# Kernel optimization log

Hardware: AMD Instinct MI355X
Metric: run time of the kernel (lower is better)

Reference implementation:

```python
import jax, jax.numpy as jnp
import numpy as np
from jax import lax

B, IMG, P, CIN = 8, 224, 16, 3
D, NH, E, HID, DEPTH, NC = 768, 12, 4, 3072, 12, 1000
NPAT = (IMG // P) ** 2  # 196
S = NPAT + 1            # 197 tokens incl cls
HD = D // NH            # 64
EPS = 1e-5


def _ln(x, g, b):
    m = jnp.mean(x, axis=-1, keepdims=True)
    v = jnp.mean((x - m) ** 2, axis=-1, keepdims=True)
    return (x - m) * lax.rsqrt(v + EPS) * g + b


def setup_inputs() -> dict:
    key = jax.random.key(0)
    ks = list(jax.random.split(key, 24))
    def rn(k, shape, s=0.02):
        return (jax.random.normal(k, shape) * s).astype(jnp.float32)
    inp = {
        "x": jax.random.normal(ks[0], (B, CIN, IMG, IMG), dtype=jnp.float32),
        "patch_w": rn(ks[1], (D, CIN, P, P)),
        "patch_b": jnp.zeros((D,), jnp.float32),
        "cls_token": jnp.zeros((1, 1, D), jnp.float32),
        "pos_embed": rn(ks[2], (1, S, D)),
        "ln1_g": jnp.ones((DEPTH, D), jnp.float32),
        "ln1_b": jnp.zeros((DEPTH, D), jnp.float32),
        "ln2_g": jnp.ones((DEPTH, D), jnp.float32),
        "ln2_b": jnp.zeros((DEPTH, D), jnp.float32),
        "attn_in_w": rn(ks[3], (DEPTH, 3 * D, D)),
        "attn_in_b": jnp.zeros((DEPTH, 3 * D), jnp.float32),
        "attn_out_w": rn(ks[4], (DEPTH, D, D)),
        "attn_out_b": jnp.zeros((DEPTH, D), jnp.float32),
        "gate_w": rn(ks[5], (DEPTH, E, D)),
        "gate_b": jnp.zeros((DEPTH, E), jnp.float32),
        "w1": rn(ks[6], (DEPTH, E, D, HID)),
        "b1": jnp.zeros((DEPTH, E, HID), jnp.float32),
        "w2": rn(ks[7], (DEPTH, E, HID, D)),
        "b2": jnp.zeros((DEPTH, E, D), jnp.float32),
        "head_w": rn(ks[8], (NC, D)),
        "head_b": jnp.zeros((NC,), jnp.float32),
    }
    return inp


def _forward(x, patch_w, patch_b, cls_token, pos_embed, ln1_g, ln1_b, ln2_g, ln2_b,
             attn_in_w, attn_in_b, attn_out_w, attn_out_b, gate_w, gate_b,
             w1, b1, w2, b2, head_w, head_b):
    # Patch embedding: conv stride=patch, then flatten spatial -> tokens
    feat = lax.conv_general_dilated(x, patch_w, window_strides=(P, P), padding="VALID",
                                    dimension_numbers=("NCHW", "OIHW", "NCHW"))
    t = feat.reshape(B, D, NPAT).transpose(0, 2, 1) + patch_b  # [B, 196, D]
    cls = jnp.broadcast_to(cls_token, (B, 1, D))
    h = jnp.concatenate([cls, t], axis=1) + pos_embed  # [B, S, D]

    scale = 1.0 / np.sqrt(HD).astype(np.float32)
    for i in range(DEPTH):
        # ---- attention (query = LN(x); key/value = x, as in source) ----
        qn = _ln(h, ln1_g[i], ln1_b[i])
        wq, wk, wv = attn_in_w[i, :D], attn_in_w[i, D:2 * D], attn_in_w[i, 2 * D:]
        bq, bk, bv = attn_in_b[i, :D], attn_in_b[i, D:2 * D], attn_in_b[i, 2 * D:]
        q = (qn @ wq.T + bq).reshape(B, S, NH, HD)
        k = (h @ wk.T + bk).reshape(B, S, NH, HD)
        v = (h @ wv.T + bv).reshape(B, S, NH, HD)
        scores = jnp.einsum("bqhd,bkhd->bhqk", q, k) * scale
        attn = jax.nn.softmax(scores, axis=-1)
        o = jnp.einsum("bhqk,bkhd->bqhd", attn, v).reshape(B, S, D)
        h = h + o @ attn_out_w[i].T + attn_out_b[i]

        # ---- Top-1 gated MoE MLP ----
        y = _ln(h, ln2_g[i], ln2_b[i])
        logits = y @ gate_w[i].T + gate_b[i]            # [B,S,E]
        probs = jax.nn.softmax(logits, axis=-1)
        top = jnp.argmax(probs, axis=-1)                # [B,S]
        onehot = jax.nn.one_hot(top, E, dtype=y.dtype)  # [B,S,E]
        gv = jnp.sum(probs * onehot, axis=-1)           # [B,S] top-1 gate score
        hidd = jax.nn.gelu(jnp.einsum("bsd,edh->besh", y, w1[i]) + b1[i][None, :, None, :])
        eout = jnp.einsum("besh,ehd->besd", hidd, w2[i]) + b2[i][None, :, None, :]
        moe = jnp.einsum("bse,besd->bsd", onehot, eout) * gv[..., None]
        h = h + moe

    return h[:, 0] @ head_w.T + head_b  # [B, NC]


def reference(x, patch_w, patch_b, cls_token, pos_embed, ln1_g, ln1_b, ln2_g, ln2_b,
              attn_in_w, attn_in_b, attn_out_w, attn_out_b, gate_w, gate_b,
              w1, b1, w2, b2, head_w, head_b):
    return _forward(x, patch_w, patch_b, cls_token, pos_embed, ln1_g, ln1_b, ln2_g,
                    ln2_b, attn_in_w, attn_in_b, attn_out_w, attn_out_b, gate_w,
                    gate_b, w1, b1, w2, b2, head_w, head_b)
```

## Files before the change

### kernel.cpp

```cpp
#include <hip/hip_runtime.h>
#include <math.h>


#define BB 8
#define SS 197
#define DD 768
#define MT (BB*SS)
#define NPATCH 196
#define MPE (BB*NPATCH)
#define HHID 3072
#define NEXP 4
#define QKVN 2304
#define SCW 228

typedef __bf16 bf16_t;
typedef bf16_t bf16x4 __attribute__((ext_vector_type(4)));
typedef bf16_t bf16x8 __attribute__((ext_vector_type(8)));
typedef float  f32x4  __attribute__((ext_vector_type(4)));

__device__ __forceinline__ void gload16(const bf16_t* g, bf16_t* l) {
    __builtin_amdgcn_global_load_lds(
        (const __attribute__((address_space(1))) unsigned int*)g,
        (__attribute__((address_space(3))) unsigned int*)l,
        16, 0, 0);
}

__device__ __forceinline__ bf16x8 cvt8(float4 a, float4 b) {
    bf16x8 o;
    o[0]=(bf16_t)a.x; o[1]=(bf16_t)a.y; o[2]=(bf16_t)a.z; o[3]=(bf16_t)a.w;
    o[4]=(bf16_t)b.x; o[5]=(bf16_t)b.y; o[6]=(bf16_t)b.z; o[7]=(bf16_t)b.w;
    return o;
}

__global__ void gather_patches(const float* __restrict__ x, bf16_t* __restrict__ Xp) {
    int i = blockIdx.x * 256 + threadIdx.x;
    if (i >= MPE * DD) return;
    int k = i % DD;
    int m = i / DD;
    int pw = k & 15, ph = (k >> 4) & 15, cin = k >> 8;
    int px = m % 14, py = (m / 14) % 14, b = m / NPATCH;
    int row = py * 16 + ph, col = px * 16 + pw;
    Xp[i] = (bf16_t)x[((size_t)(b * 3 + cin) * 224 + row) * 224 + col];
}

__global__ void init_misc(const float* __restrict__ cls, const float* __restrict__ pos,
                          float* __restrict__ h, bf16_t* __restrict__ hb, int* __restrict__ cnt) {
    int i = blockIdx.x * 256 + threadIdx.x;
    if (i < 12*NEXP) cnt[i] = 0;
    if (i < BB * DD) {
        int b = i / DD, d = i % DD;
        float v = cls[d] + pos[d];
        size_t o = (size_t)(b * SS) * DD + d;
        h[o] = v;
        hb[o] = (bf16_t)v;
    }
}

template<int BM, int BN, int WM, int WN, int MODE, int BL>
__global__ __launch_bounds__((BM/WM)*(BN/WN)*64) void gemm_bf16(
    const bf16_t* __restrict__ A, const bf16_t* __restrict__ A2, int nsplit,
    const float* __restrict__ Bw,
    const float* __restrict__ bias, float* __restrict__ C, bf16_t* __restrict__ Cb,
    const int* __restrict__ cnt, const int* __restrict__ idx,
    const float* __restrict__ gv, int M, int N, int K)
{
    constexpr int NW  = (BM/WM)*(BN/WN);
    constexpr int NTH = NW * 64;
    constexpr int WNC = BN/WN;
    constexpr int MI  = WM/16;
    constexpr int NI  = WN/16;
    constexpr int IA  = (BM/8)/NW;
    constexpr int BT  = (BN*8)/NTH;
    constexpr bool GATHER = (MODE == 3 || MODE == 4);

    int z = blockIdx.z;
    int count = GATHER ? cnt[z] : M;
    int m0 = blockIdx.y * BM;
    if (m0 >= count) return;
    int n0 = blockIdx.x * BN;
    if (n0 >= nsplit) A = A2;
    Bw += (size_t)z * N * K;
    const float* biasz = bias ? (bias + (size_t)z * N) : nullptr;

    __shared__ bf16_t As[2][BM * 64];
    __shared__ bf16_t Bs[2][BN * 64];
    __shared__ int toks[BM];

    int tid = threadIdx.x, lane = tid & 63, w = tid >> 6;
    if (tid < BM) {
        int mm = m0 + tid;
        if (mm > count - 1) mm = count - 1;
        toks[tid] = GATHER ? idx[z * MT + mm] : mm;
    }
    __syncthreads();

    int wm = (w / WNC) * WM, wn = (w % WNC) * WN;
    int fr = lane & 15, fs = lane >> 4;

    f32x4 acc[MI][NI];
    #pragma unroll
    for (int mi = 0; mi < MI; mi++)
        #pragma unroll
        for (int ni = 0; ni < NI; ni++)
            #pragma unroll
            for (int j = 0; j < 4; j++) acc[mi][ni][j] = 0.f;

    int nk = K >> 6;
    int srow = lane >> 3, scc = lane & 7;

    float4 bA[BT], bB[BT];
    float  bt[BT][8];

    #define A_STAGE(buf, k0)                                                            \
        {                                                                               \
            _Pragma("unroll")                                                           \
            for (int i = 0; i < IA; i++) {                                              \
                int blk = i*NW + w;                                                     \
                int row = blk*8 + srow;                                                 \
                const bf16_t* s = A + (size_t)toks[row] * K + (k0) + ((scc ^ (row & 7)) << 3); \
                gload16(s, &As[buf][blk * 512]);                                        \
            }                                                                           \
        }

    #define B_LOAD(k0)                                                                  \
        {                                                                               \
            _Pragma("unroll")                                                           \
            for (int i = 0; i < BT; i++) {                                              \
                int task = i*NTH + tid;                                                 \
                if (BL == 0) {                                                          \
                    int row = task >> 3, sl = task & 7;                                 \
                    const float* s = Bw + (size_t)(n0 + row) * K + (k0) + sl*8;         \
                    bA[i] = *(const float4*)s;                                          \
                    bB[i] = *(const float4*)(s + 4);                                    \
                } else {                                                                \
                    int n = task & (BN-1), sl = task / BN;                              \
                    const float* s = Bw + (size_t)((k0) + sl*8) * N + n0 + n;           \
                    _Pragma("unroll")                                                   \
                    for (int j = 0; j < 8; j++) bt[i][j] = s[(size_t)j * N];            \
                }                                                                       \
            }                                                                           \
        }

    #define B_WRITE(buf)                                                                \
        {                                                                               \
            _Pragma("unroll")                                                           \
            for (int i = 0; i < BT; i++) {                                              \
                int task = i*NTH + tid;                                                 \
                int row, sl;                                                            \
                bf16x8 o;                                                               \
                if (BL == 0) {                                                          \
                    row = task >> 3; sl = task & 7;                                     \
                    o = cvt8(bA[i], bB[i]);                                             \
                } else {                                                                \
                    row = task & (BN-1); sl = task / BN;                                \
                    _Pragma("unroll")                                                   \
                    for (int j = 0; j < 8; j++) o[j] = (bf16_t)bt[i][j];                \
                }                                                                       \
                *(bf16x8*)&Bs[buf][row * 64 + ((sl ^ (row & 7)) << 3)] = o;             \
            }                                                                           \
        }

    A_STAGE(0, 0);
    B_LOAD(0);
    B_WRITE(0);
    __syncthreads();
    int cur = 0;
    for (int t = 0; t < nk; t++) {
        if (t + 1 < nk) { A_STAGE(cur ^ 1, (t + 1) << 6); B_LOAD((t + 1) << 6); }
        #pragma unroll
        for (int ks = 0; ks < 2; ks++) {
            bf16x8 af[MI], bfr[NI];
            #pragma unroll
            for (int mi = 0; mi < MI; mi++) {
                int r = wm + mi * 16 + fr;
                af[mi] = *(bf16x8*)&As[cur][r * 64 + (((fs + ks*4) ^ (r & 7)) << 3)];
            }
            #pragma unroll
            for (int ni = 0; ni < NI; ni++) {
                int r = wn + ni * 16 + fr;
                bfr[ni] = *(bf16x8*)&Bs[cur][r * 64 + (((fs + ks*4) ^ (r & 7)) << 3)];
            }
            #pragma unroll
            for (int mi = 0; mi < MI; mi++)
                #pragma unroll
                for (int ni = 0; ni < NI; ni++)
                    acc[mi][ni] = __builtin_amdgcn_mfma_f32_16x16x32_bf16(af[mi], bfr[ni], acc[mi][ni], 0, 0, 0);
        }
        if (t + 1 < nk) B_WRITE(cur ^ 1);
        __syncthreads();
        cur ^= 1;
    }
    #undef A_STAGE
    #undef B_LOAD
    #undef B_WRITE

    #pragma unroll
    for (int mi = 0; mi < MI; mi++) {
        #pragma unroll
        for (int j = 0; j < 4; j++) {
            int rr = wm + mi * 16 + fs * 4 + j;
            if (m0 + rr >= count) continue;
            int crow = toks[rr];
            #pragma unroll
            for (int ni = 0; ni < NI; ni++) {
                int col = n0 + wn + ni * 16 + fr;
                float v = acc[mi][ni][j];
                if (MODE >= 2) v += biasz[col];
                if (MODE == 2) {
                    C[(size_t)crow * N + col] += v;
                } else if (MODE == 3) {
                    float g = 0.5f * v * (1.0f + tanhf(0.7978845608028654f * (v + 0.044715f * v * v * v)));
                    Cb[(size_t)crow * N + col] = (bf16_t)g;
                } else if (MODE == 4) {
                    float* p = &C[(size_t)crow * N + col];
                    float nv = *p + v * gv[crow];
                    *p = nv;
                    Cb[(size_t)crow * N + col] = (bf16_t)nv;
                } else if (MODE == 5) {
                    Cb[(size_t)crow * N + col] = (bf16_t)v;
                } else if (MODE == 7) {
                    int bb = crow / NPATCH, p = crow - bb * NPATCH;
                    size_t o = ((size_t)(bb * SS + 1 + p)) * DD + col;
                    float vv = v + gv[(size_t)(1 + p) * DD + col];
                    C[o] = vv;
                    Cb[o] = (bf16_t)vv;
                }
            }
        }
    }
}

__global__ __launch_bounds__(256) void ln1_kernel(const float* __restrict__ x,
                                                  const float* __restrict__ g,
                                                  const float* __restrict__ b,
                                                  bf16_t* __restrict__ qn)
{
    int wid = (blockIdx.x * 256 + threadIdx.x) >> 6;
    if (wid >= MT) return;
    int lane = threadIdx.x & 63;
    const float4* xr = (const float4*)(x + (size_t)wid * DD);
    float4 v0 = xr[lane], v1 = xr[lane + 64], v2 = xr[lane + 128];
    float s = v0.x+v0.y+v0.z+v0.w + v1.x+v1.y+v1.z+v1.w + v2.x+v2.y+v2.z+v2.w;
    #pragma unroll
    for (int o = 32; o > 0; o >>= 1) s += __shfl_xor(s, o);
    float mean = s * (1.0f/DD);
    float s2 = 0.f;
    #pragma unroll
    for (int c = 0; c < 3; c++) {
        float4 v = c == 0 ? v0 : (c == 1 ? v1 : v2);
        float dx = v.x-mean, dy = v.y-mean, dz = v.z-mean, dw = v.w-mean;
        s2 += dx*dx + dy*dy + dz*dz + dw*dw;
    }
    #pragma unroll
    for (int o = 32; o > 0; o >>= 1) s2 += __shfl_xor(s2, o);
    float rs = rsqrtf(s2 * (1.0f/DD) + 1e-5f);
    const float4* gr = (const float4*)g;
    const float4* br = (const float4*)b;
    #pragma unroll
    for (int c = 0; c < 3; c++) {
        float4 v = c == 0 ? v0 : (c == 1 ? v1 : v2);
        float4 gg = gr[lane + 64*c], bb = br[lane + 64*c];
        bf16x4 o;
        o[0] = (bf16_t)((v.x - mean) * rs * gg.x + bb.x);
        o[1] = (bf16_t)((v.y - mean) * rs * gg.y + bb.y);
        o[2] = (bf16_t)((v.z - mean) * rs * gg.z + bb.z);
        o[3] = (bf16_t)((v.w - mean) * rs * gg.w + bb.w);
        *(bf16x4*)(qn + (size_t)wid * DD + (lane + 64*c) * 4) = o;
    }
}

__global__ __launch_bounds__(256) void ln2_gate_kernel(const float* __restrict__ x,
                                                       const float* __restrict__ g,
                                                       const float* __restrict__ b,
                                                       const float* __restrict__ gw,
                                                       const float* __restrict__ gb,
                                                       bf16_t* __restrict__ yb,
                                                       float* __restrict__ gv,
                                                       int* __restrict__ cnt,
                                                       int* __restrict__ idxb)
{
    int wid = (blockIdx.x * 256 + threadIdx.x) >> 6;
    if (wid >= MT) return;
    int lane = threadIdx.x & 63;
    const float4* xr = (const float4*)(x + (size_t)wid * DD);
    float4 v0 = xr[lane], v1 = xr[lane + 64], v2 = xr[lane + 128];
    float s = v0.x+v0.y+v0.z+v0.w + v1.x+v1.y+v1.z+v1.w + v2.x+v2.y+v2.z+v2.w;
    #pragma unroll
    for (int o = 32; o > 0; o >>= 1) s += __shfl_xor(s, o);
    float mean = s * (1.0f/DD);
    float s2 = 0.f;
    #pragma unroll
    for (int c = 0; c < 3; c++) {
        float4 v = c == 0 ? v0 : (c == 1 ? v1 : v2);
        float dx = v.x-mean, dy = v.y-mean, dz = v.z-mean, dw = v.w-mean;
        s2 += dx*dx + dy*dy + dz*dz + dw*dw;
    }
    #pragma unroll
    for (int o = 32; o > 0; o >>= 1) s2 += __shfl_xor(s2, o);
    float rs = rsqrtf(s2 * (1.0f/DD) + 1e-5f);
    const float4* gr = (const float4*)g;
    const float4* br = (const float4*)b;
    float p0 = 0.f, p1 = 0.f, p2 = 0.f, p3 = 0.f;
    #pragma unroll
    for (int c = 0; c < 3; c++) {
        float4 v = c == 0 ? v0 : (c == 1 ? v1 : v2);
        float4 gg = gr[lane + 64*c], bb = br[lane + 64*c];
        float y0 = (v.x - mean) * rs * gg.x + bb.x;
        float y1 = (v.y - mean) * rs * gg.y + bb.y;
        float y2 = (v.z - mean) * rs * gg.z + bb.z;
        float y3 = (v.w - mean) * rs * gg.w + bb.w;
        bf16x4 o; o[0]=(bf16_t)y0; o[1]=(bf16_t)y1; o[2]=(bf16_t)y2; o[3]=(bf16_t)y3;
        *(bf16x4*)(yb + (size_t)wid * DD + (lane + 64*c) * 4) = o;
        int off = lane + 64*c;
        float4 w0 = ((const float4*)(gw          ))[off];
        float4 w1v = ((const float4*)(gw +   DD  ))[off];
        float4 w2v = ((const float4*)(gw + 2*DD  ))[off];
        float4 w3v = ((const float4*)(gw + 3*DD  ))[off];
        p0 += y0*w0.x + y1*w0.y + y2*w0.z + y3*w0.w;
        p1 += y0*w1v.x + y1*w1v.y + y2*w1v.z + y3*w1v.w;
        p2 += y0*w2v.x + y1*w2v.y + y2*w2v.z + y3*w2v.w;
        p3 += y0*w3v.x + y1*w3v.y + y2*w3v.z + y3*w3v.w;
    }
    #pragma unroll
    for (int o = 32; o > 0; o >>= 1) {
        p0 += __shfl_xor(p0, o); p1 += __shfl_xor(p1, o);
        p2 += __shfl_xor(p2, o); p3 += __shfl_xor(p3, o);
    }
    if (lane == 0) {
        float l0 = p0 + gb[0], l1 = p1 + gb[1], l2 = p2 + gb[2], l3 = p3 + gb[3];
        int top = 0; float best = l0;
        if (l1 > best) { best = l1; top = 1; }
        if (l2 > best) { best = l2; top = 2; }
        if (l3 > best) { best = l3; top = 3; }
        float Z = __expf(l0-best) + __expf(l1-best) + __expf(l2-best) + __expf(l3-best);
        gv[wid] = 1.0f / Z;
        int pos = atomicAdd(&cnt[top], 1);
        idxb[top * MT + pos] = wid;
    }
}

__global__ __launch_bounds__(256) void attn_kernel(const bf16_t* __restrict__ qkv,
                                                   bf16_t* __restrict__ ob)
{
    int qt = blockIdx.x, hh = blockIdx.y, b = blockIdx.z;
    __shared__ bf16_t Qs[64 * 64];
    __shared__ bf16_t KV[64 * 68];
    __shared__ float  Sc[64 * SCW];
    __shared__ float  linv[64];

    int tid = threadIdx.x, lane = tid & 63, w = tid >> 6;
    int wm = (w >> 1) * 32, wn = (w & 1) * 32;
    int fr = lane & 15, fs = lane >> 4;

    #pragma unroll
    for (int it = 0; it < 2; it++) {
        int row = 8*(it*4 + w) + (lane >> 3), cc = lane & 7;
        int q = qt*64 + row; if (q > SS-1) q = SS-1;
        const bf16_t* src = qkv + ((size_t)(b*SS + q))*QKVN + hh*64 + ((cc ^ (row & 7)) << 3);
        gload16(src, &Qs[(it*4 + w) * 512]);
    }

    for (int kt = 0; kt < 4; kt++) {
        __syncthreads();
        #pragma unroll
        for (int it = 0; it < 2; it++) {
            int row = 8*(it*4 + w) + (lane >> 3), cc = lane & 7;
            int k = kt*64 + row; if (k > SS-1) k = SS-1;
            const bf16_t* src = qkv + ((size_t)(b*SS + k))*QKVN + 768 + hh*64 + ((cc ^ (row & 7)) << 3);
            gload16(src, &KV[(it*4 + w) * 512]);
        }
        __syncthreads();
        f32x4 acc[2][2];
        #pragma unroll
        for (int mi = 0; mi < 2; mi++)
            #pragma unroll
            for (int ni = 0; ni < 2; ni++)
                #pragma unroll
                for (int j = 0; j < 4; j++) acc[mi][ni][j] = 0.f;
        #pragma unroll
        for (int ks = 0; ks < 2; ks++) {
            bf16x8 af[2], bfr[2];
            #pragma unroll
            for (int mi = 0; mi < 2; mi++) {
                int r = wm + mi * 16 + fr;
                af[mi] = *(bf16x8*)&Qs[r * 64 + (((fs + ks*4) ^ (r & 7)) << 3)];
            }
            #pragma unroll
            for (int ni = 0; ni < 2; ni++) {
                int r = wn + ni * 16 + fr;
                bfr[ni] = *(bf16x8*)&KV[r * 64 + (((fs + ks*4) ^ (r & 7)) << 3)];
            }
            #pragma unroll
            for (int mi = 0; mi < 2; mi++)
                #pragma unroll
                for (int ni = 0; ni < 2; ni++)
                    acc[mi][ni] = __builtin_amdgcn_mfma_f32_16x16x32_bf16(af[mi], bfr[ni], acc[mi][ni], 0, 0, 0);
        }
        #pragma unroll
        for (int mi = 0; mi < 2; mi++)
            #pragma unroll
            for (int j = 0; j < 4; j++) {
                int qr = wm + mi * 16 + fs * 4 + j;
                #pragma unroll
                for (int ni = 0; ni < 2; ni++) {
                    int col = kt*64 + wn + ni * 16 + fr;
                    if (col < SCW) {
                        float v = acc[mi][ni][j] * 0.125f;
                        if (col > SS-1) v = -1e30f;
                        Sc[qr * SCW + col] = v;
                    }
                }
            }
    }
    __syncthreads();

    {
        int row = tid >> 2, c = tid & 3;
        float m = -1e30f;
        for (int i = c; i < SCW; i += 4) m = fmaxf(m, Sc[row * SCW + i]);
        m = fmaxf(m, __shfl_xor(m, 1, 4));
        m = fmaxf(m, __shfl_xor(m, 2, 4));
        float s = 0.f;
        for (int i = c; i < SCW; i += 4) {
            float e = __expf(Sc[row * SCW + i] - m);
            Sc[row * SCW + i] = e;
            s += e;
        }
        s += __shfl_xor(s, 1, 4);
        s += __shfl_xor(s, 2, 4);
        if (c == 0) linv[row] = 1.0f / s;
    }

    f32x4 pv[2][2];
    #pragma unroll
    for (int mi = 0; mi < 2; mi++)
        #pragma unroll
        for (int ni = 0; ni < 2; ni++)
            #pragma unroll
            for (int j = 0; j < 4; j++) pv[mi][ni][j] = 0.f;

    for (int kt = 0; kt < 4; kt++) {
        __syncthreads();
        {
            int s = tid >> 2, c2 = tid & 3;
            int k = kt*64 + s; if (k > SS-1) k = SS-1;
            const bf16_t* vr = qkv + ((size_t)(b*SS + k))*QKVN + 1536 + hh*64;
            bf16x8 v0 = *(const bf16x8*)(vr + c2*16);
            bf16x8 v1 = *(const bf16x8*)(vr + c2*16 + 8);
            #pragma unroll
            for (int j = 0; j < 8; j++) {
                KV[(c2*16 + j) * 68 + s]     = v0[j];
                KV[(c2*16 + 8 + j) * 68 + s] = v1[j];
            }
        }
        __syncthreads();
        #pragma unroll
        for (int ks = 0; ks < 2; ks++) {
            int s0 = kt*64 + ks*32;
            if (s0 > SS-1) continue;
            bf16x8 af[2], bfr[2];
            #pragma unroll
            for (int mi = 0; mi < 2; mi++) {
                int qr = wm + mi * 16 + fr;
                const float* p = &Sc[qr * SCW + s0 + fs * 8];
                af[mi] = cvt8(*(const float4*)p, *(const float4*)(p + 4));
            }
            #pragma unroll
            for (int ni = 0; ni < 2; ni++) {
                int d = wn + ni * 16 + fr;
                bfr[ni] = *(bf16x8*)&KV[d * 68 + ks*32 + fs*8];
            }
            #pragma unroll
            for (int mi = 0; mi < 2; mi++)
                #pragma unroll
                for (int ni = 0; ni < 2; ni++)
                    pv[mi][ni] = __builtin_amdgcn_mfma_f32_16x16x32_bf16(af[mi], bfr[ni], pv[mi][ni], 0, 0, 0);
        }
    }

    #pragma unroll
    for (int mi = 0; mi < 2; mi++)
        #pragma unroll
        for (int j = 0; j < 4; j++) {
            int qr = wm + mi * 16 + fs * 4 + j;
            int q = qt*64 + qr;
            if (q > SS-1) continue;
            float il = linv[qr];
            #pragma unroll
            for (int ni = 0; ni < 2; ni++) {
                int d = wn + ni * 16 + fr;
                ob[((size_t)(b*SS + q))*DD + hh*64 + d] = (bf16_t)(pv[mi][ni][j] * il);
            }
        }
}

__global__ void head_kernel(const float* __restrict__ h, const float* __restrict__ hw,
                            const float* __restrict__ hb, float* __restrict__ out)
{
    int i = blockIdx.x * 256 + threadIdx.x;
    if (i >= BB * 1000) return;
    int b = i & 7, n = i >> 3;
    const float4* hr = (const float4*)(h + (size_t)(b * SS) * DD);
    const float4* wr = (const float4*)(hw + (size_t)n * DD);
    float s = 0.f;
    #pragma unroll 4
    for (int k = 0; k < DD/4; k++) {
        float4 a = hr[k], wv = wr[k];
        s += a.x*wv.x + a.y*wv.y + a.z*wv.z + a.w*wv.w;
    }
    out[b * 1000 + n] = s + hb[n];
}

extern "C" void kernel_launch(void* const* d_in, const int* in_sizes, int n_in,
                              void* d_out, int out_size, void* d_ws, size_t ws_size,
                              hipStream_t stream) {
    const float* x          = (const float*)d_in[0];
    const float* patch_w    = (const float*)d_in[1];
    const float* patch_b    = (const float*)d_in[2];
    const float* cls_token  = (const float*)d_in[3];
    const float* pos_embed  = (const float*)d_in[4];
    const float* ln1_g      = (const float*)d_in[5];
    const float* ln1_b      = (const float*)d_in[6];
    const float* ln2_g      = (const float*)d_in[7];
    const float* ln2_b      = (const float*)d_in[8];
    const float* attn_in_w  = (const float*)d_in[9];
    const float* attn_in_b  = (const float*)d_in[10];
    const float* attn_out_w = (const float*)d_in[11];
    const float* attn_out_b = (const float*)d_in[12];
    const float* gate_w     = (const float*)d_in[13];
    const float* gate_b     = (const float*)d_in[14];
    const float* w1         = (const float*)d_in[15];
    const float* b1         = (const float*)d_in[16];
    const float* w2         = (const float*)d_in[17];
    const float* b2         = (const float*)d_in[18];
    const float* head_w     = (const float*)d_in[19];
    const float* head_b     = (const float*)d_in[20];
    float* out = (float*)d_out;

    char* wsb = (char*)d_ws;
    auto alloc = [&](size_t bytes) { char* p = wsb; wsb += (bytes + 63) & ~63ULL; return p; };
    bf16_t* Xp     = (bf16_t*)alloc((size_t)MPE * DD * 2);
    float*  h      = (float*) alloc((size_t)MT * DD * 4);
    bf16_t* qn_bf  = (bf16_t*)alloc((size_t)MT * DD * 2);
    bf16_t* h_bf   = (bf16_t*)alloc((size_t)MT * DD * 2);
    bf16_t* qkv_bf = (bf16_t*)alloc((size_t)MT * QKVN * 2);
    bf16_t* ob_bf  = (bf16_t*)alloc((size_t)MT * DD * 2);
    bf16_t* yb_bf  = (bf16_t*)alloc((size_t)MT * DD * 2);
    bf16_t* hd_bf  = (bf16_t*)alloc((size_t)MT * HHID * 2);
    float*  gv     = (float*) alloc((size_t)MT * 4);
    int*    cnt    = (int*)   alloc(12 * NEXP * 4);
    int*    idxb   = (int*)   alloc((size_t)12 * NEXP * MT * 4);

    dim3 blk(256);
    dim3 blk512(512);
    const int NOSPLIT = 1 << 30;

    init_misc<<<24, blk, 0, stream>>>(cls_token, pos_embed, h, h_bf, cnt);
    gather_patches<<<(MPE*DD + 255)/256, blk, 0, stream>>>(x, Xp);
    gemm_bf16<64,64,32,32,7,0><<<dim3(12, 25, 1), blk, 0, stream>>>(
        Xp, nullptr, NOSPLIT, patch_w, patch_b, h, h_bf, nullptr, nullptr, pos_embed, MPE, DD, DD);

    for (int i = 0; i < 12; i++) {
        const float* aw    = attn_in_w  + (size_t)i * QKVN * DD;
        const float* ow    = attn_out_w + (size_t)i * DD * DD;
        const float* w1l   = w1 + (size_t)i * NEXP * DD * HHID;
        const float* w2l   = w2 + (size_t)i * NEXP * HHID * DD;
        const float* ab    = attn_in_b  + (size_t)i * QKVN;
        const float* obias = attn_out_b + (size_t)i * DD;
        const float* l1g = ln1_g + (size_t)i * DD;
        const float* l1b = ln1_b + (size_t)i * DD;
        const float* l2g = ln2_g + (size_t)i * DD;
        const float* l2b = ln2_b + (size_t)i * DD;
        const float* gw  = gate_w + (size_t)i * NEXP * DD;
        const float* gb  = gate_b + (size_t)i * NEXP;
        const float* b1l = b1 + (size_t)i * NEXP * HHID;
        const float* b2l = b2 + (size_t)i * NEXP * DD;
        int* cnt_i  = cnt  + i * NEXP;
        int* idxb_i = idxb + (size_t)i * NEXP * MT;

        ln1_kernel<<<dim3((MT*64 + 255)/256), blk, 0, stream>>>(h, l1g, l1b, qn_bf);
        gemm_bf16<128,64,64,32,5,0><<<dim3(QKVN/64, 13, 1), blk, 0, stream>>>(
            qn_bf, h_bf, DD, aw, ab, nullptr, qkv_bf, nullptr, nullptr, nullptr, MT, QKVN, DD);
        attn_kernel<<<dim3(4, 12, BB), blk, 0, stream>>>(qkv_bf, ob_bf);
        gemm_bf16<64,64,32,32,2,0><<<dim3(12, 25, 1), blk, 0, stream>>>(
            ob_bf, nullptr, NOSPLIT, ow, obias, h, nullptr, nullptr, nullptr, nullptr, MT, DD, DD);
        ln2_gate_kernel<<<dim3((MT*64 + 255)/256), blk, 0, stream>>>(
            h, l2g, l2b, gw, gb, yb_bf, gv, cnt_i, idxb_i);
        gemm_bf16<128,128,64,32,3,1><<<dim3(HHID/128, 13, NEXP), blk512, 0, stream>>>(
            yb_bf, nullptr, NOSPLIT, w1l, b1l, nullptr, hd_bf, cnt_i, idxb_i, nullptr, MT, HHID, DD);
        gemm_bf16<64,64,32,32,4,1><<<dim3(12, 25, NEXP), blk, 0, stream>>>(
            hd_bf, nullptr, NOSPLIT, w2l, b2l, h, h_bf, cnt_i, idxb_i, gv, MT, DD, HHID);
    }

    head_kernel<<<(BB*1000 + 255)/256, blk, 0, stream>>>(h, head_w, head_b, out);
}
```

Baseline: 2.139 ms.

## Fuse LayerNorm-1 into QKV GEMM A-load using precomputed row stats

```diff
diff --git a/kernel.cpp b/kernel.cpp
--- a/kernel.cpp
+++ b/kernel.cpp
@@ -43,26 +43,46 @@
     Xp[i] = (bf16_t)x[((size_t)(b * 3 + cin) * 224 + row) * 224 + col];
 }
 
-__global__ void init_misc(const float* __restrict__ cls, const float* __restrict__ pos,
-                          float* __restrict__ h, bf16_t* __restrict__ hb, int* __restrict__ cnt) {
+__global__ void zero_cnt(int* __restrict__ cnt) {
+    int i = threadIdx.x;
+    if (i < 12*NEXP) cnt[i] = 0;
+}
+
+__global__ void init_cls(const float* __restrict__ cls, const float* __restrict__ pos,
+                         float* __restrict__ h) {
     int i = blockIdx.x * 256 + threadIdx.x;
-    if (i < 12*NEXP) cnt[i] = 0;
-    if (i < BB * DD) {
-        int b = i / DD, d = i % DD;
-        float v = cls[d] + pos[d];
-        size_t o = (size_t)(b * SS) * DD + d;
-        h[o] = v;
-        hb[o] = (bf16_t)v;
-    }
-}
-
-template<int BM, int BN, int WM, int WN, int MODE, int BL>
+    if (i >= BB * DD) return;
+    int b = i / DD, d = i % DD;
+    h[(size_t)(b * SS) * DD + d] = cls[d] + pos[d];
+}
+
+__global__ __launch_bounds__(256) void row_stats(const float* __restrict__ x,
+                                                 float* __restrict__ rs,
+                                                 float* __restrict__ rq) {
+    int wid = (blockIdx.x * 256 + threadIdx.x) >> 6;
+    if (wid >= MT) return;
+    int lane = threadIdx.x & 63;
+    const float4* xr = (const float4*)(x + (size_t)wid * DD);
+    float4 v0 = xr[lane], v1 = xr[lane + 64], v2 = xr[lane + 128];
+    float s = v0.x+v0.y+v0.z+v0.w + v1.x+v1.y+v1.z+v1.w + v2.x+v2.y+v2.z+v2.w;
+    float q = v0.x*v0.x+v0.y*v0.y+v0.z*v0.z+v0.w*v0.w
+            + v1.x*v1.x+v1.y*v1.y+v1.z*v1.z+v1.w*v1.w
+            + v2.x*v2.x+v2.y*v2.y+v2.z*v2.z+v2.w*v2.w;
+    #pragma unroll
+    for (int o = 32; o > 0; o >>= 1) { s += __shfl_xor(s, o); q += __shfl_xor(q, o); }
+    if (lane == 0) { rs[wid] = s; rq[wid] = q; }
+}
+
+template<int BM, int BN, int WM, int WN, int MODE, int BL, int ALN>
 __global__ __launch_bounds__((BM/WM)*(BN/WN)*64) void gemm_bf16(
-    const bf16_t* __restrict__ A, const bf16_t* __restrict__ A2, int nsplit,
+    const void* __restrict__ Av, int nsplit,
     const float* __restrict__ Bw,
     const float* __restrict__ bias, float* __restrict__ C, bf16_t* __restrict__ Cb,
     const int* __restrict__ cnt, const int* __restrict__ idx,
-    const float* __restrict__ gv, int M, int N, int K)
+    const float* __restrict__ gv,
+    const float* __restrict__ lng, const float* __restrict__ lnb,
+    const float* __restrict__ rsumG, const float* __restrict__ rsqG,
+    int M, int N, int K)
 {
     constexpr int NW  = (BM/WM)*(BN/WN);
     constexpr int NTH = NW * 64;
@@ -70,6 +90,7 @@
     constexpr int MI  = WM/16;
     constexpr int NI  = WN/16;
     constexpr int IA  = (BM/8)/NW;
+    constexpr int AT  = (BM*8)/NTH;
     constexpr int BT  = (BN*8)/NTH;
     constexpr bool GATHER = (MODE == 3 || MODE == 4);
 
@@ -78,7 +99,9 @@
     int m0 = blockIdx.y * BM;
     if (m0 >= count) return;
     int n0 = blockIdx.x * BN;
-    if (n0 >= nsplit) A = A2;
+    const bf16_t* A  = (ALN == 0) ? (const bf16_t*)Av : nullptr;
+    const float*  Ah = (ALN == 1) ? (const float*)Av  : nullptr;
+    bool doLN = (ALN == 1) && (n0 < nsplit);
     Bw += (size_t)z * N * K;
     const float* biasz = bias ? (bias + (size_t)z * N) : nullptr;
 
@@ -108,8 +131,24 @@
     int nk = K >> 6;
     int srow = lane >> 3, scc = lane & 7;
 
-    float4 bA[BT], bB[BT];
+    float4 wA[BT], wB[BT];
     float  bt[BT][8];
+    float4 xA[AT], xB[AT];
+    float4 gA[AT], gB[AT], bA4[AT], bB4[AT];
+    float  meanT[AT], rsT[AT];
+
+    if (ALN == 1 && doLN) {
+        #pragma unroll
+        for (int i = 0; i < AT; i++) {
+            int ar = (i*NTH + tid) >> 3;
+            int tk = toks[ar];
+            float s = rsumG[tk], q = rsqG[tk];
+            float m = s * (1.0f/DD);
+            float v = q * (1.0f/DD) - m*m;
+            meanT[i] = m;
+            rsT[i] = rsqrtf(v + 1e-5f);
+        }
+    }
 
     #define A_STAGE(buf, k0)                                                            \
         {                                                                               \
@@ -122,6 +161,46 @@
             }                                                                           \
         }
 
+    #define A_LOAD_LN(k0)                                                               \
+        {                                                                               \
+            _Pragma("unroll")                                                           \
+            for (int i = 0; i < AT; i++) {                                              \
+                int task = i*NTH + tid;                                                 \
+                int ar = task >> 3, sl = task & 7;                                      \
+                const float* s = Ah + (size_t)toks[ar] * K + (k0) + sl*8;               \
+                xA[i] = *(const float4*)s;                                              \
+                xB[i] = *(const float4*)(s + 4);                                        \
+                if (doLN) {                                                             \
+                    gA[i]  = *(const float4*)(lng + (k0) + sl*8);                       \
+                    gB[i]  = *(const float4*)(lng + (k0) + sl*8 + 4);                   \
+                    bA4[i] = *(const float4*)(lnb + (k0) + sl*8);                       \
+                    bB4[i] = *(const float4*)(lnb + (k0) + sl*8 + 4);                   \
+                }                                                                       \
+            }                                                                           \
+        }
+
+    #define A_WRITE_LN(buf)                                                             \
+        {                                                                               \
+            _Pragma("unroll")                                                           \
+            for (int i = 0; i < AT; i++) {                                              \
+                int task = i*NTH + tid;                                                 \
+                int ar = task >> 3, sl = task & 7;                                      \
+                float4 p0 = xA[i], p1 = xB[i];                                          \
+                if (doLN) {                                                             \
+                    float m = meanT[i], r = rsT[i];                                     \
+                    p0.x = (p0.x - m)*r*gA[i].x + bA4[i].x;                             \
+                    p0.y = (p0.y - m)*r*gA[i].y + bA4[i].y;                             \
+                    p0.z = (p0.z - m)*r*gA[i].z + bA4[i].z;                             \
+                    p0.w = (p0.w - m)*r*gA[i].w + bA4[i].w;                             \
+                    p1.x = (p1.x - m)*r*gB[i].x + bB4[i].x;                             \
+                    p1.y = (p1.y - m)*r*gB[i].y + bB4[i].y;                             \
+                    p1.z = (p1.z - m)*r*gB[i].z + bB4[i].z;                             \
+                    p1.w = (p1.w - m)*r*gB[i].w + bB4[i].w;                             \
+                }                                                                       \
+                *(bf16x8*)&As[buf][ar * 64 + ((sl ^ (ar & 7)) << 3)] = cvt8(p0, p1);    \
+            }                                                                           \
+        }
+
     #define B_LOAD(k0)                                                                  \
         {                                                                               \
             _Pragma("unroll")                                                           \
@@ -130,8 +209,8 @@
                 if (BL == 0) {                                                          \
                     int row = task >> 3, sl = task & 7;                                 \
                     const float* s = Bw + (size_t)(n0 + row) * K + (k0) + sl*8;         \
-                    bA[i] = *(const float4*)s;                                          \
-                    bB[i] = *(const float4*)(s + 4);                                    \
+                    wA[i] = *(const float4*)s;                                          \
+                    wB[i] = *(const float4*)(s + 4);                                    \
                 } else {                                                                \
                     int n = task & (BN-1), sl = task / BN;                              \
                     const float* s = Bw + (size_t)((k0) + sl*8) * N + n0 + n;           \
@@ -150,7 +229,7 @@
                 bf16x8 o;                                                               \
                 if (BL == 0) {                                                          \
                     row = task >> 3; sl = task & 7;                                     \
-                    o = cvt8(bA[i], bB[i]);                                             \
+                    o = cvt8(wA[i], wB[i]);                                             \
                 } else {                                                                \
                     row = task & (BN-1); sl = task / BN;                                \
                     _Pragma("unroll")                                                   \
@@ -160,13 +239,17 @@
             }                                                                           \
         }
 
-    A_STAGE(0, 0);
+    if (ALN == 1) { A_LOAD_LN(0); } else { A_STAGE(0, 0); }
     B_LOAD(0);
+    if (ALN == 1) { A_WRITE_LN(0); }
     B_WRITE(0);
     __syncthreads();
     int cur = 0;
     for (int t = 0; t < nk; t++) {
-        if (t + 1 < nk) { A_STAGE(cur ^ 1, (t + 1) << 6); B_LOAD((t + 1) << 6); }
+        if (t + 1 < nk) {
+            if (ALN == 1) { A_LOAD_LN((t + 1) << 6); } else { A_STAGE(cur ^ 1, (t + 1) << 6); }
+            B_LOAD((t + 1) << 6);
+        }
         #pragma unroll
         for (int ks = 0; ks < 2; ks++) {
             bf16x8 af[MI], bfr[NI];
@@ -186,11 +269,16 @@
                 for (int ni = 0; ni < NI; ni++)
                     acc[mi][ni] = __builtin_amdgcn_mfma_f32_16x16x32_bf16(af[mi], bfr[ni], acc[mi][ni], 0, 0, 0);
         }
-        if (t + 1 < nk) B_WRITE(cur ^ 1);
+        if (t + 1 < nk) {
+            if (ALN == 1) { A_WRITE_LN(cur ^ 1); }
+            B_WRITE(cur ^ 1);
+        }
         __syncthreads();
         cur ^= 1;
     }
     #undef A_STAGE
+    #undef A_LOAD_LN
+    #undef A_WRITE_LN
     #undef B_LOAD
     #undef B_WRITE
 
@@ -212,60 +300,16 @@
                     float g = 0.5f * v * (1.0f + tanhf(0.7978845608028654f * (v + 0.044715f * v * v * v)));
                     Cb[(size_t)crow * N + col] = (bf16_t)g;
                 } else if (MODE == 4) {
-                    float* p = &C[(size_t)crow * N + col];
-                    float nv = *p + v * gv[crow];
-                    *p = nv;
-                    Cb[(size_t)crow * N + col] = (bf16_t)nv;
+                    C[(size_t)crow * N + col] += v * gv[crow];
                 } else if (MODE == 5) {
                     Cb[(size_t)crow * N + col] = (bf16_t)v;
                 } else if (MODE == 7) {
                     int bb = crow / NPATCH, p = crow - bb * NPATCH;
                     size_t o = ((size_t)(bb * SS + 1 + p)) * DD + col;
-                    float vv = v + gv[(size_t)(1 + p) * DD + col];
-                    C[o] = vv;
-                    Cb[o] = (bf16_t)vv;
+                    C[o] = v + gv[(size_t)(1 + p) * DD + col];
                 }
             }
         }
-    }
-}
-
-__global__ __launch_bounds__(256) void ln1_kernel(const float* __restrict__ x,
-                                                  const float* __restrict__ g,
-                                                  const float* __restrict__ b,
-                                                  bf16_t* __restrict__ qn)
-{
-    int wid = (blockIdx.x * 256 + threadIdx.x) >> 6;
-    if (wid >= MT) return;
-    int lane = threadIdx.x & 63;
-    const float4* xr = (const float4*)(x + (size_t)wid * DD);
-    float4 v0 = xr[lane], v1 = xr[lane + 64], v2 = xr[lane + 128];
-    float s = v0.x+v0.y+v0.z+v0.w + v1.x+v1.y+v1.z+v1.w + v2.x+v2.y+v2.z+v2.w;
-    #pragma unroll
-    for (int o = 32; o > 0; o >>= 1) s += __shfl_xor(s, o);
-    float mean = s * (1.0f/DD);
-    float s2 = 0.f;
-    #pragma unroll
-    for (int c = 0; c < 3; c++) {
-        float4 v = c == 0 ? v0 : (c == 1 ? v1 : v2);
-        float dx = v.x-mean, dy = v.y-mean, dz = v.z-mean, dw = v.w-mean;
-        s2 += dx*dx + dy*dy + dz*dz + dw*dw;
-    }
-    #pragma unroll
-    for (int o = 32; o > 0; o >>= 1) s2 += __shfl_xor(s2, o);
-    float rs = rsqrtf(s2 * (1.0f/DD) + 1e-5f);
-    const float4* gr = (const float4*)g;
-    const float4* br = (const float4*)b;
-    #pragma unroll
-    for (int c = 0; c < 3; c++) {
-        float4 v = c == 0 ? v0 : (c == 1 ? v1 : v2);
-        float4 gg = gr[lane + 64*c], bb = br[lane + 64*c];
-        bf16x4 o;
-        o[0] = (bf16_t)((v.x - mean) * rs * gg.x + bb.x);
-        o[1] = (bf16_t)((v.y - mean) * rs * gg.y + bb.y);
-        o[2] = (bf16_t)((v.z - mean) * rs * gg.z + bb.z);
-        o[3] = (bf16_t)((v.w - mean) * rs * gg.w + bb.w);
-        *(bf16x4*)(qn + (size_t)wid * DD + (lane + 64*c) * 4) = o;
     }
 }
 
@@ -297,7 +341,7 @@
     }
     #pragma unroll
     for (int o = 32; o > 0; o >>= 1) s2 += __shfl_xor(s2, o);
-    float rs = rsqrtf(s2 * (1.0f/DD) + 1e-5f);
+    float rsv = rsqrtf(s2 * (1.0f/DD) + 1e-5f);
     const float4* gr = (const float4*)g;
     const float4* br = (const float4*)b;
     float p0 = 0.f, p1 = 0.f, p2 = 0.f, p3 = 0.f;
@@ -305,10 +349,10 @@
     for (int c = 0; c < 3; c++) {
         float4 v = c == 0 ? v0 : (c == 1 ? v1 : v2);
         float4 gg = gr[lane + 64*c], bb = br[lane + 64*c];
-        float y0 = (v.x - mean) * rs * gg.x + bb.x;
-        float y1 = (v.y - mean) * rs * gg.y + bb.y;
-        float y2 = (v.z - mean) * rs * gg.z + bb.z;
-        float y3 = (v.w - mean) * rs * gg.w + bb.w;
+        float y0 = (v.x - mean) * rsv * gg.x + bb.x;
+        float y1 = (v.y - mean) * rsv * gg.y + bb.y;
+        float y2 = (v.z - mean) * rsv * gg.z + bb.z;
+        float y3 = (v.w - mean) * rsv * gg.w + bb.w;
         bf16x4 o; o[0]=(bf16_t)y0; o[1]=(bf16_t)y1; o[2]=(bf16_t)y2; o[3]=(bf16_t)y3;
         *(bf16x4*)(yb + (size_t)wid * DD + (lane + 64*c) * 4) = o;
         int off = lane + 64*c;
@@ -541,13 +585,13 @@
     auto alloc = [&](size_t bytes) { char* p = wsb; wsb += (bytes + 63) & ~63ULL; return p; };
     bf16_t* Xp     = (bf16_t*)alloc((size_t)MPE * DD * 2);
     float*  h      = (float*) alloc((size_t)MT * DD * 4);
-    bf16_t* qn_bf  = (bf16_t*)alloc((size_t)MT * DD * 2);
-    bf16_t* h_bf   = (bf16_t*)alloc((size_t)MT * DD * 2);
     bf16_t* qkv_bf = (bf16_t*)alloc((size_t)MT * QKVN * 2);
     bf16_t* ob_bf  = (bf16_t*)alloc((size_t)MT * DD * 2);
     bf16_t* yb_bf  = (bf16_t*)alloc((size_t)MT * DD * 2);
     bf16_t* hd_bf  = (bf16_t*)alloc((size_t)MT * HHID * 2);
     float*  gv     = (float*) alloc((size_t)MT * 4);
+    float*  rsum   = (float*) alloc((size_t)MT * 4);
+    float*  rsq    = (float*) alloc((size_t)MT * 4);
     int*    cnt    = (int*)   alloc(12 * NEXP * 4);
     int*    idxb   = (int*)   alloc((size_t)12 * NEXP * MT * 4);
 
@@ -555,10 +599,12 @@
     dim3 blk512(512);
     const int NOSPLIT = 1 << 30;
 
-    init_misc<<<24, blk, 0, stream>>>(cls_token, pos_embed, h, h_bf, cnt);
+    zero_cnt<<<1, 64, 0, stream>>>(cnt);
+    init_cls<<<(BB*DD + 255)/256, blk, 0, stream>>>(cls_token, pos_embed, h);
     gather_patches<<<(MPE*DD + 255)/256, blk, 0, stream>>>(x, Xp);
-    gemm_bf16<64,64,32,32,7,0><<<dim3(12, 25, 1), blk, 0, stream>>>(
-        Xp, nullptr, NOSPLIT, patch_w, patch_b, h, h_bf, nullptr, nullptr, pos_embed, MPE, DD, DD);
+    gemm_bf16<64,64,32,32,7,0,0><<<dim3(12, 25, 1), blk, 0, stream>>>(
+        Xp, NOSPLIT, patch_w, patch_b, h, nullptr, nullptr, nullptr, pos_embed,
+        nullptr, nullptr, nullptr, nullptr, MPE, DD, DD);
 
     for (int i = 0; i < 12; i++) {
         const float* aw    = attn_in_w  + (size_t)i * QKVN * DD;
@@ -578,18 +624,22 @@
         int* cnt_i  = cnt  + i * NEXP;
         int* idxb_i = idxb + (size_t)i * NEXP * MT;
 
-        ln1_kernel<<<dim3((MT*64 + 255)/256), blk, 0, stream>>>(h, l1g, l1b, qn_bf);
-        gemm_bf16<128,64,64,32,5,0><<<dim3(QKVN/64, 13, 1), blk, 0, stream>>>(
-            qn_bf, h_bf, DD, aw, ab, nullptr, qkv_bf, nullptr, nullptr, nullptr, MT, QKVN, DD);
+        row_stats<<<dim3((MT*64 + 255)/256), blk, 0, stream>>>(h, rsum, rsq);
+        gemm_bf16<128,64,64,32,5,0,1><<<dim3(QKVN/64, 13, 1), blk, 0, stream>>>(
+            h, DD, aw, ab, nullptr, qkv_bf, nullptr, nullptr, nullptr,
+            l1g, l1b, rsum, rsq, MT, QKVN, DD);
         attn_kernel<<<dim3(4, 12, BB), blk, 0, stream>>>(qkv_bf, ob_bf);
-        gemm_bf16<64,64,32,32,2,0><<<dim3(12, 25, 1), blk, 0, stream>>>(
-            ob_bf, nullptr, NOSPLIT, ow, obias, h, nullptr, nullptr, nullptr, nullptr, MT, DD, DD);
+        gemm_bf16<64,64,32,32,2,0,0><<<dim3(12, 25, 1), blk, 0, stream>>>(
+            ob_bf, NOSPLIT, ow, obias, h, nullptr, nullptr, nullptr, nullptr,
+            nullptr, nullptr, nullptr, nullptr, MT, DD, DD);
         ln2_gate_kernel<<<dim3((MT*64 + 255)/256), blk, 0, stream>>>(
             h, l2g, l2b, gw, gb, yb_bf, gv, cnt_i, idxb_i);
-        gemm_bf16<128,128,64,32,3,1><<<dim3(HHID/128, 13, NEXP), blk512, 0, stream>>>(
-            yb_bf, nullptr, NOSPLIT, w1l, b1l, nullptr, hd_bf, cnt_i, idxb_i, nullptr, MT, HHID, DD);
-        gemm_bf16<64,64,32,32,4,1><<<dim3(12, 25, NEXP), blk, 0, stream>>>(
-            hd_bf, nullptr, NOSPLIT, w2l, b2l, h, h_bf, cnt_i, idxb_i, gv, MT, DD, HHID);
+        gemm_bf16<128,128,64,32,3,1,0><<<dim3(HHID/128, 13, NEXP), blk512, 0, stream>>>(
+            yb_bf, NOSPLIT, w1l, b1l, nullptr, hd_bf, cnt_i, idxb_i, nullptr,
+            nullptr, nullptr, nullptr, nullptr, MT, HHID, DD);
+        gemm_bf16<64,64,32,32,4,1,0><<<dim3(12, 25, NEXP), blk, 0, stream>>>(
+            hd_bf, NOSPLIT, w2l, b2l, h, nullptr, cnt_i, idxb_i, gv,
+            nullptr, nullptr, nullptr, nullptr, MT, DD, HHID);
     }
 
     head_kernel<<<(BB*1000 + 255)/256, blk, 0, stream>>>(h, head_w, head_b, out);
```

Result: slower. 2.260 ms (+5.6%).
